# Optimization experiments

Hardware: AMD Instinct MI355X
Metric: run time of the kernel (lower is better)

## Reference

```python
import jax, jax.numpy as jnp
import numpy as np

HEAD_NUM = 8
EMB_SIZE = 768
B, N = 8, 1024


def setup_inputs() -> dict:
    key = jax.random.key(0)
    ks = jax.random.split(key, 9)
    s = 0.02
    return {
        "x": jax.random.normal(ks[0], (B, N, EMB_SIZE), dtype=jnp.float32),
        "Wq": jax.random.normal(ks[1], (EMB_SIZE, EMB_SIZE), dtype=jnp.float32) * s,
        "bq": jax.random.normal(ks[2], (EMB_SIZE,), dtype=jnp.float32) * s,
        "Wk": jax.random.normal(ks[3], (EMB_SIZE, EMB_SIZE), dtype=jnp.float32) * s,
        "bk": jax.random.normal(ks[4], (EMB_SIZE,), dtype=jnp.float32) * s,
        "Wv": jax.random.normal(ks[5], (EMB_SIZE, EMB_SIZE), dtype=jnp.float32) * s,
        "bv": jax.random.normal(ks[6], (EMB_SIZE,), dtype=jnp.float32) * s,
        "Wp": jax.random.normal(ks[7], (EMB_SIZE, EMB_SIZE), dtype=jnp.float32) * s,
        "bp": jax.random.normal(ks[8], (EMB_SIZE,), dtype=jnp.float32) * s,
    }


def reference(x, Wq, bq, Wk, bk, Wv, bv, Wp, bp):
    b, n, e = x.shape
    h = HEAD_NUM
    d = e // h
    # nn.Linear: y = x @ W^T + b
    q = (x @ Wq.T + bq).reshape(b, h, n, d)  # NOTE: raw reshape, as in source
    k = (x @ Wk.T + bk).reshape(b, h, n, d)
    v = (x @ Wv.T + bv).reshape(b, h, n, d)
    energy = jnp.einsum('bhqd,bhkd->bhqk', q, k)
    # source divides by sqrt(emb_size) AFTER softmax (faithful)
    attn = jax.nn.softmax(energy, axis=-1) / jnp.sqrt(jnp.float32(e))
    out = jnp.einsum('bhql,bhld->bhqd', attn, v).reshape(b, n, h * d)
    return out @ Wp.T + bp
```

## Files before the change

### kernel.cpp

```cpp
#include <hip/hip_runtime.h>
#include <hip/hip_bf16.h>


typedef __attribute__((ext_vector_type(8))) short short8;
typedef __attribute__((ext_vector_type(4))) float floatx4;
typedef __attribute__((ext_vector_type(16))) float floatx16;

static constexpr int EMB = 768;
static constexpr int SEQ = 1024;
static constexpr int DH = 96;
static constexpr int NBH = 64;
static constexpr int HEADBLK = SEQ * DH;
static constexpr int MROWS = 8192;
static constexpr int NW = EMB * EMB;
static constexpr int QKVN = 3 * EMB;

__device__ __forceinline__ unsigned bfround(float f) {
    unsigned u = __builtin_bit_cast(unsigned, f);
    return u + 0x7FFFu + ((u >> 16) & 1u);
}
__device__ __forceinline__ unsigned short f2bf(float f) {
    return (unsigned short)(bfround(f) >> 16);
}
__device__ __forceinline__ unsigned pk2(float lo, float hi) {
    return (bfround(lo) >> 16) | (bfround(hi) & 0xFFFF0000u);
}

__device__ __forceinline__ void gload16(const unsigned short* g, unsigned short* l) {
    __builtin_amdgcn_global_load_lds(
        (const __attribute__((address_space(1))) unsigned int*)g,
        (__attribute__((address_space(3))) unsigned int*)l, 16, 0, 0);
}

__global__ void cast_all(const float* __restrict__ x,
                         const float* __restrict__ Wq, const float* __restrict__ Wk,
                         const float* __restrict__ Wv, const float* __restrict__ Wp,
                         const float* __restrict__ bq, const float* __restrict__ bk,
                         const float* __restrict__ bv,
                         unsigned short* __restrict__ xb,
                         unsigned short* __restrict__ Wqkv, unsigned short* __restrict__ Wpb,
                         float* __restrict__ bias) {
    int bx = blockIdx.x;
    if (bx < 6144) {
        int i = bx * 1024 + threadIdx.x * 4;
        float4 v = *reinterpret_cast<const float4*>(x + i);
        ushort4 o;
        o.x = f2bf(v.x); o.y = f2bf(v.y); o.z = f2bf(v.z); o.w = f2bf(v.w);
        *reinterpret_cast<ushort4*>(xb + i) = o;
    } else if (bx < 8448) {
        int i4 = (bx - 6144) * 1024 + threadIdx.x * 4;
        const float* src;
        unsigned short* dst;
        if (i4 < 3 * NW) {
            int wi = i4 / NW;
            src = (wi == 0) ? Wq + i4 : (wi == 1) ? Wk + (i4 - NW) : Wv + (i4 - 2 * NW);
            dst = Wqkv + i4;
        } else {
            src = Wp + (i4 - 3 * NW);
            dst = Wpb + (i4 - 3 * NW);
        }
        float4 v = *reinterpret_cast<const float4*>(src);
        ushort4 o;
        o.x = f2bf(v.x); o.y = f2bf(v.y); o.z = f2bf(v.z); o.w = f2bf(v.w);
        *reinterpret_cast<ushort4*>(dst) = o;
    } else {
        int j = (bx - 8448) * 256 + threadIdx.x;
        if (j < QKVN)
            bias[j] = (j < 768) ? bq[j] : (j < 1536) ? bk[j - 768] : bv[j - 1536];
    }
}

__global__ __launch_bounds__(256) void gemm_qkv(
    const unsigned short* __restrict__ A,
    const unsigned short* __restrict__ Bm,
    const float* __restrict__ bias,
    unsigned short* __restrict__ Qo,
    unsigned short* __restrict__ Ko,
    unsigned short* __restrict__ Vo) {
    __shared__ unsigned short As[128 * 64];
    __shared__ unsigned short Bs[128 * 64];
    const int K = EMB;

    const int t = threadIdx.x;
    const int lane = t & 63;
    const int w = t >> 6;
    const int wm = (w >> 1) * 64;
    const int wn = (w & 1) * 64;
    const int l32 = lane & 31;
    const int lh = lane >> 5;
    const int bm = blockIdx.x * 128;
    const int by = blockIdx.y;
    const int bn = by * 128;

    const unsigned short* Agp[4];
    const unsigned short* Bgp[4];
#pragma unroll
    for (int i = 0; i < 4; i++) {
        int f = i * 2048 + w * 512 + lane * 8;
        int row = f >> 6;
        int cc = (f >> 3) & 7;
        int gk = (cc ^ (row & 7)) * 8;
        Agp[i] = A + (size_t)(bm + row) * K + gk;
        Bgp[i] = Bm + (size_t)(bn + row) * K + gk;
    }

    floatx16 acc[2][2];
#pragma unroll
    for (int i = 0; i < 2; i++)
#pragma unroll
        for (int j = 0; j < 2; j++)
#pragma unroll
            for (int r = 0; r < 16; r++) acc[i][j][r] = 0.0f;

    const int sx = lane & 7;
    for (int k0 = 0; k0 < K; k0 += 64) {
        __syncthreads();
#pragma unroll
        for (int i = 0; i < 4; i++) {
            gload16(Agp[i] + k0, As + i * 2048 + w * 512);
            gload16(Bgp[i] + k0, Bs + i * 2048 + w * 512);
        }
        __syncthreads();

#pragma unroll
        for (int ks = 0; ks < 4; ks++) {
            const int co = ((ks * 2 + lh) ^ sx) * 8;
            short8 af[2], bfr[2];
#pragma unroll
            for (int mt = 0; mt < 2; mt++)
                af[mt] = *reinterpret_cast<const short8*>(As + (wm + mt * 32 + l32) * 64 + co);
#pragma unroll
            for (int nt = 0; nt < 2; nt++)
                bfr[nt] = *reinterpret_cast<const short8*>(Bs + (wn + nt * 32 + l32) * 64 + co);
#pragma unroll
            for (int mt = 0; mt < 2; mt++)
#pragma unroll
                for (int nt = 0; nt < 2; nt++)
                    acc[mt][nt] = __builtin_amdgcn_mfma_f32_32x32x16_bf16(af[mt], bfr[nt], acc[mt][nt], 0, 0, 0);
        }
    }

    unsigned short* dst = (by < 6) ? Qo : (by < 12) ? Ko : Vo;
    const int bnl = (by % 6) * 128;
#pragma unroll
    for (int mt = 0; mt < 2; mt++) {
#pragma unroll
        for (int nt = 0; nt < 2; nt++) {
            int colg = bn + wn + nt * 32 + l32;
            int coll = bnl + wn + nt * 32 + l32;
            float bb = bias[colg];
#pragma unroll
            for (int rg = 0; rg < 4; rg++) {
                int rowb = bm + wm + mt * 32 + rg * 8 + lh * 4;
#pragma unroll
                for (int rr = 0; rr < 4; rr++)
                    dst[(size_t)(rowb + rr) * EMB + coll] = f2bf(acc[mt][nt][rg * 4 + rr] + bb);
            }
        }
    }
}

__global__ __launch_bounds__(256) void gemm_proj(
    const unsigned short* __restrict__ A,
    const unsigned short* __restrict__ Bm,
    const float* __restrict__ bias,
    float* __restrict__ C) {
    __shared__ unsigned short As[64 * 64];
    __shared__ unsigned short Bs[128 * 64];
    const int K = EMB, N = EMB;

    const int t = threadIdx.x;
    const int lane = t & 63;
    const int w = t >> 6;
    const int wm = (w >> 1) * 32;
    const int wn = (w & 1) * 64;
    const int l32 = lane & 31;
    const int lh = lane >> 5;
    const int bm = blockIdx.x * 64;
    const int bn = blockIdx.y * 128;

    const unsigned short* Agp[2];
    const unsigned short* Bgp[4];
#pragma unroll
    for (int i = 0; i < 2; i++) {
        int f = i * 2048 + w * 512 + lane * 8;
        int row = f >> 6;
        int cc = (f >> 3) & 7;
        Agp[i] = A + (size_t)(bm + row) * K + ((cc ^ (row & 7)) * 8);
    }
#pragma unroll
    for (int i = 0; i < 4; i++) {
        int f = i * 2048 + w * 512 + lane * 8;
        int row = f >> 6;
        int cc = (f >> 3) & 7;
        Bgp[i] = Bm + (size_t)(bn + row) * K + ((cc ^ (row & 7)) * 8);
    }

    floatx16 acc[2];
#pragma unroll
    for (int j = 0; j < 2; j++)
#pragma unroll
        for (int r = 0; r < 16; r++) acc[j][r] = 0.0f;

    const int sx = lane & 7;
    for (int k0 = 0; k0 < K; k0 += 64) {
        __syncthreads();
#pragma unroll
        for (int i = 0; i < 2; i++) gload16(Agp[i] + k0, As + i * 2048 + w * 512);
#pragma unroll
        for (int i = 0; i < 4; i++) gload16(Bgp[i] + k0, Bs + i * 2048 + w * 512);
        __syncthreads();

#pragma unroll
        for (int ks = 0; ks < 4; ks++) {
            const int co = ((ks * 2 + lh) ^ sx) * 8;
            short8 af = *reinterpret_cast<const short8*>(As + (wm + l32) * 64 + co);
            short8 bfr[2];
#pragma unroll
            for (int nt = 0; nt < 2; nt++)
                bfr[nt] = *reinterpret_cast<const short8*>(Bs + (wn + nt * 32 + l32) * 64 + co);
#pragma unroll
            for (int nt = 0; nt < 2; nt++)
                acc[nt] = __builtin_amdgcn_mfma_f32_32x32x16_bf16(af, bfr[nt], acc[nt], 0, 0, 0);
        }
    }

#pragma unroll
    for (int nt = 0; nt < 2; nt++) {
        int col = bn + wn + nt * 32 + l32;
        float bb = bias[col];
#pragma unroll
        for (int rg = 0; rg < 4; rg++) {
            int rowb = bm + wm + rg * 8 + lh * 4;
#pragma unroll
            for (int rr = 0; rr < 4; rr++)
                C[(size_t)(rowb + rr) * N + col] = acc[nt][rg * 4 + rr] + bb;
        }
    }
}

__global__ __launch_bounds__(256) void transpose_v(const unsigned short* __restrict__ V,
                                                   unsigned short* __restrict__ Vt) {
    __shared__ unsigned short L[64 * 104];
    const int t = threadIdx.x;
    const int bh = blockIdx.x, nb = blockIdx.y;
    const unsigned short* Vg = V + (size_t)bh * HEADBLK + (size_t)nb * 64 * DH;
#pragma unroll
    for (int i = 0; i < 3; i++) {
        int f = i * 2048 + t * 8;
        int r = f / 96, c = f - r * 96;
        *reinterpret_cast<short8*>(L + r * 104 + c) = *reinterpret_cast<const short8*>(Vg + f);
    }
    __syncthreads();
    unsigned short* dst = Vt + (size_t)bh * HEADBLK;
#pragma unroll
    for (int i = 0; i < 3; i++) {
        int f = i * 2048 + t * 8;
        int d = f >> 6, c0 = f & 63;
        union { short8 s; unsigned short u[8]; } o;
#pragma unroll
        for (int j = 0; j < 8; j++) {
            int c = c0 + j;
            int key = (c & ~12) | ((c & 4) << 1) | ((c & 8) >> 1);
            o.u[j] = L[key * 104 + d];
        }
        *reinterpret_cast<short8*>(dst + d * SEQ + nb * 64 + c0) = o.s;
    }
}

__global__ __launch_bounds__(256, 2) void attn_kernel(
    const unsigned short* __restrict__ Q,
    const unsigned short* __restrict__ K,
    const unsigned short* __restrict__ Vt,
    unsigned short* __restrict__ O) {
    __shared__ unsigned short Ks[64 * 104];
    __shared__ unsigned short Vs[96 * 72];

    const int t = threadIdx.x;
    const int lane = t & 63;
    const int w = t >> 6;
    const int l32 = lane & 31;
    const int lh = lane >> 5;
    const int bh = blockIdx.x, qb = blockIdx.y;

    const unsigned short* Qh = Q + (size_t)bh * HEADBLK;
    const unsigned short* Kh = K + (size_t)bh * HEADBLK;
    const unsigned short* Vth = Vt + (size_t)bh * HEADBLK;

    short8 qf[6];
    {
        const unsigned short* qsrc = Qh + (size_t)(qb * 128 + w * 32 + l32) * DH + lh * 8;
#pragma unroll
        for (int ks = 0; ks < 6; ks++)
            qf[ks] = *reinterpret_cast<const short8*>(qsrc + ks * 16);
    }

    const unsigned short* Kp[3];
    const unsigned short* Vp[3];
    unsigned short* KsW[3];
    unsigned short* VsW[3];
#pragma unroll
    for (int i = 0; i < 3; i++) {
        int f = i * 2048 + t * 8;
        int r = f / 96, c = f - r * 96;
        Kp[i] = Kh + f;
        KsW[i] = Ks + r * 104 + c;
        int d = f >> 6, cv = f & 63;
        Vp[i] = Vth + d * SEQ + cv;
        VsW[i] = Vs + d * 72 + cv;
    }

    short8 kreg[3], vreg[3];
#pragma unroll
    for (int i = 0; i < 3; i++) {
        kreg[i] = *reinterpret_cast<const short8*>(Kp[i]);
        vreg[i] = *reinterpret_cast<const short8*>(Vp[i]);
    }

    float l_ = 0.0f;
    floatx16 acco[3];
#pragma unroll
    for (int n = 0; n < 3; n++)
#pragma unroll
        for (int r = 0; r < 16; r++) acco[n][r] = 0.0f;

    for (int kb = 0; kb < 16; kb++) {
        __syncthreads();
#pragma unroll
        for (int i = 0; i < 3; i++) {
            *reinterpret_cast<short8*>(KsW[i]) = kreg[i];
            *reinterpret_cast<short8*>(VsW[i]) = vreg[i];
        }
        __syncthreads();
        if (kb < 15) {
#pragma unroll
            for (int i = 0; i < 3; i++) {
                kreg[i] = *reinterpret_cast<const short8*>(Kp[i] + (kb + 1) * 6144);
                vreg[i] = *reinterpret_cast<const short8*>(Vp[i] + (kb + 1) * 64);
            }
        }

        floatx16 sacc[2];
#pragma unroll
        for (int kt = 0; kt < 2; kt++)
#pragma unroll
            for (int r = 0; r < 16; r++) sacc[kt][r] = 0.0f;

#pragma unroll
        for (int ks = 0; ks < 6; ks++) {
#pragma unroll
            for (int kt = 0; kt < 2; kt++) {
                short8 ak = *reinterpret_cast<const short8*>(
                    Ks + (kt * 32 + l32) * 104 + ks * 16 + lh * 8);
                sacc[kt] = __builtin_amdgcn_mfma_f32_32x32x16_bf16(ak, qf[ks], sacc[kt], 0, 0, 0);
            }
        }

        float rs = 0.0f;
#pragma unroll
        for (int kt = 0; kt < 2; kt++)
#pragma unroll
            for (int r = 0; r < 16; r++) {
                float v = __expf(sacc[kt][r]);
                sacc[kt][r] = v;
                rs += v;
            }
        rs += __shfl_xor(rs, 32);
        l_ += rs;

#pragma unroll
        for (int kt2 = 0; kt2 < 4; kt2++) {
            const int kt = kt2 >> 1, ro = (kt2 & 1) * 8;
            union { short8 s8; unsigned u[4]; } bp;
#pragma unroll
            for (int p = 0; p < 4; p++)
                bp.u[p] = pk2(sacc[kt][ro + 2 * p], sacc[kt][ro + 2 * p + 1]);
#pragma unroll
            for (int n = 0; n < 3; n++) {
                short8 av = *reinterpret_cast<const short8*>(
                    Vs + (n * 32 + l32) * 72 + kt2 * 16 + lh * 8);
                acco[n] = __builtin_amdgcn_mfma_f32_32x32x16_bf16(av, bp.s8, acco[n], 0, 0, 0);
            }
        }
    }

    const float inv_sqrt_e = 0.036084391824351615f;
    float invl = inv_sqrt_e / l_;
    unsigned short* dst = O + (size_t)bh * HEADBLK +
                          (size_t)(qb * 128 + w * 32 + l32) * DH + lh * 4;
#pragma unroll
    for (int n = 0; n < 3; n++) {
#pragma unroll
        for (int rg = 0; rg < 4; rg++) {
            uint2 o2;
            o2.x = pk2(acco[n][rg * 4 + 0] * invl, acco[n][rg * 4 + 1] * invl);
            o2.y = pk2(acco[n][rg * 4 + 2] * invl, acco[n][rg * 4 + 3] * invl);
            *reinterpret_cast<uint2*>(dst + n * 32 + rg * 8) = o2;
        }
    }
}

extern "C" void kernel_launch(void* const* d_in, const int* in_sizes, int n_in,
                              void* d_out, int out_size, void* d_ws, size_t ws_size,
                              hipStream_t stream) {
    const float* x = (const float*)d_in[0];
    const float* Wq = (const float*)d_in[1];
    const float* bq = (const float*)d_in[2];
    const float* Wk = (const float*)d_in[3];
    const float* bk = (const float*)d_in[4];
    const float* Wv = (const float*)d_in[5];
    const float* bv = (const float*)d_in[6];
    const float* Wp = (const float*)d_in[7];
    const float* bp = (const float*)d_in[8];
    float* out = (float*)d_out;

    char* ws = (char*)d_ws;
    size_t off = 0;
    auto alloc = [&](size_t bytes) {
        char* p = ws + off;
        off += (bytes + 255) & ~(size_t)255;
        return p;
    };
    const int nx = MROWS * EMB;
    unsigned short* xb    = (unsigned short*)alloc((size_t)nx * 2);
    unsigned short* Wqkvb = (unsigned short*)alloc((size_t)3 * NW * 2);
    unsigned short* Wpb   = (unsigned short*)alloc((size_t)NW * 2);
    float*          biasq = (float*)alloc((size_t)QKVN * 4);
    unsigned short* Qb    = (unsigned short*)alloc((size_t)nx * 2);
    unsigned short* Kb    = (unsigned short*)alloc((size_t)nx * 2);
    unsigned short* Vb    = (unsigned short*)alloc((size_t)nx * 2);
    unsigned short* Vtb   = (unsigned short*)alloc((size_t)nx * 2);
    unsigned short* Ob    = (unsigned short*)alloc((size_t)nx * 2);

    cast_all<<<8457, 256, 0, stream>>>(x, Wq, Wk, Wv, Wp, bq, bk, bv,
                                       xb, Wqkvb, Wpb, biasq);

    gemm_qkv<<<dim3(MROWS / 128, QKVN / 128), 256, 0, stream>>>(
        xb, Wqkvb, biasq, Qb, Kb, Vb);

    transpose_v<<<dim3(NBH, SEQ / 64), 256, 0, stream>>>(Vb, Vtb);

    attn_kernel<<<dim3(NBH, SEQ / 128), 256, 0, stream>>>(Qb, Kb, Vtb, Ob);

    gemm_proj<<<dim3(MROWS / 64, EMB / 128), 256, 0, stream>>>(Ob, Wpb, bp, out);
}
```

Before: 188.7 us.

## Triple-buffer QKV GEMM with async global-to-LDS loads and 128x256 tiles

Rewrites the QKV projection GEMM to use 512-thread blocks computing 128x256 output tiles, with a three-stage LDS ring fed by asynchronous global loads two k-steps ahead. Explicit vmcnt waits plus one barrier per step replace the old two-barrier load-then-compute loop. All fragments of a k-step are loaded before an MFMA burst issued at raised priority. The aim is to hide global latency and reduce sync overhead, at the cost of a larger LDS footprint (about 144KB per block) and higher register pressure, which can limit occupancy.

```diff
diff --git a/kernel.cpp b/kernel.cpp
--- a/kernel.cpp
+++ b/kernel.cpp
@@ -70,38 +70,40 @@
     }
 }
 
-__global__ __launch_bounds__(256) void gemm_qkv(
+__global__ __launch_bounds__(512, 2) void gemm_qkv(
     const unsigned short* __restrict__ A,
     const unsigned short* __restrict__ Bm,
     const float* __restrict__ bias,
     unsigned short* __restrict__ Qo,
     unsigned short* __restrict__ Ko,
     unsigned short* __restrict__ Vo) {
-    __shared__ unsigned short As[128 * 64];
-    __shared__ unsigned short Bs[128 * 64];
-    const int K = EMB;
+    __shared__ unsigned short lds[3 * 24576];
 
     const int t = threadIdx.x;
     const int lane = t & 63;
     const int w = t >> 6;
-    const int wm = (w >> 1) * 64;
-    const int wn = (w & 1) * 64;
+    const int wm = (w >> 2) * 64;
+    const int wn = (w & 3) * 64;
     const int l32 = lane & 31;
     const int lh = lane >> 5;
+    const int sx = l32 & 7;
     const int bm = blockIdx.x * 128;
     const int by = blockIdx.y;
-    const int bn = by * 128;
-
-    const unsigned short* Agp[4];
+    const int bn = by * 256;
+
+    const unsigned short* Agp[2];
     const unsigned short* Bgp[4];
 #pragma unroll
+    for (int i = 0; i < 2; i++) {
+        int f = i * 512 + w * 64 + lane;
+        int row = f >> 3, cc = f & 7;
+        Agp[i] = A + (size_t)(bm + row) * EMB + ((cc ^ (row & 7)) * 8);
+    }
+#pragma unroll
     for (int i = 0; i < 4; i++) {
-        int f = i * 2048 + w * 512 + lane * 8;
-        int row = f >> 6;
-        int cc = (f >> 3) & 7;
-        int gk = (cc ^ (row & 7)) * 8;
-        Agp[i] = A + (size_t)(bm + row) * K + gk;
-        Bgp[i] = Bm + (size_t)(bn + row) * K + gk;
+        int f = i * 512 + w * 64 + lane;
+        int row = f >> 3, cc = f & 7;
+        Bgp[i] = Bm + (size_t)(bn + row) * EMB + ((cc ^ (row & 7)) * 8);
     }
 
     floatx16 acc[2][2];
@@ -112,36 +114,61 @@
 #pragma unroll
             for (int r = 0; r < 16; r++) acc[i][j][r] = 0.0f;
 
-    const int sx = lane & 7;
-    for (int k0 = 0; k0 < K; k0 += 64) {
-        __syncthreads();
-#pragma unroll
-        for (int i = 0; i < 4; i++) {
-            gload16(Agp[i] + k0, As + i * 2048 + w * 512);
-            gload16(Bgp[i] + k0, Bs + i * 2048 + w * 512);
-        }
-        __syncthreads();
-
+    auto stage = [&](int tt, int b) {
+        unsigned short* Ab = lds + b * 24576;
+        unsigned short* Bb = Ab + 8192;
+        const int ko = tt * 64;
+#pragma unroll
+        for (int i = 0; i < 2; i++)
+            gload16(Agp[i] + ko, Ab + i * 4096 + w * 512);
+#pragma unroll
+        for (int i = 0; i < 4; i++)
+            gload16(Bgp[i] + ko, Bb + i * 4096 + w * 512);
+    };
+
+    stage(0, 0);
+    stage(1, 1);
+
+#pragma unroll
+    for (int tt = 0; tt < 12; tt++) {
+        if (tt == 11) {
+            asm volatile("s_waitcnt vmcnt(0)" ::: "memory");
+        } else {
+            asm volatile("s_waitcnt vmcnt(6)" ::: "memory");
+        }
+        __builtin_amdgcn_s_barrier();
+        __builtin_amdgcn_sched_barrier(0);
+        if (tt + 2 < 12) stage(tt + 2, (tt + 2) % 3);
+
+        const unsigned short* Ab = lds + (tt % 3) * 24576;
+        const unsigned short* Bb = Ab + 8192;
+        short8 af[4][2], bfq[4][2];
 #pragma unroll
         for (int ks = 0; ks < 4; ks++) {
             const int co = ((ks * 2 + lh) ^ sx) * 8;
-            short8 af[2], bfr[2];
 #pragma unroll
             for (int mt = 0; mt < 2; mt++)
-                af[mt] = *reinterpret_cast<const short8*>(As + (wm + mt * 32 + l32) * 64 + co);
+                af[ks][mt] = *reinterpret_cast<const short8*>(
+                    Ab + (wm + mt * 32 + l32) * 64 + co);
 #pragma unroll
             for (int nt = 0; nt < 2; nt++)
-                bfr[nt] = *reinterpret_cast<const short8*>(Bs + (wn + nt * 32 + l32) * 64 + co);
+                bfq[ks][nt] = *reinterpret_cast<const short8*>(
+                    Bb + (wn + nt * 32 + l32) * 64 + co);
+        }
+        __builtin_amdgcn_s_setprio(1);
+#pragma unroll
+        for (int ks = 0; ks < 4; ks++)
 #pragma unroll
             for (int mt = 0; mt < 2; mt++)
 #pragma unroll
                 for (int nt = 0; nt < 2; nt++)
-                    acc[mt][nt] = __builtin_amdgcn_mfma_f32_32x32x16_bf16(af[mt], bfr[nt], acc[mt][nt], 0, 0, 0);
-        }
-    }
-
-    unsigned short* dst = (by < 6) ? Qo : (by < 12) ? Ko : Vo;
-    const int bnl = (by % 6) * 128;
+                    acc[mt][nt] = __builtin_amdgcn_mfma_f32_32x32x16_bf16(
+                        af[ks][mt], bfq[ks][nt], acc[mt][nt], 0, 0, 0);
+        __builtin_amdgcn_s_setprio(0);
+    }
+
+    unsigned short* dst = (by < 3) ? Qo : (by < 6) ? Ko : Vo;
+    const int bnl = (by % 3) * 256;
 #pragma unroll
     for (int mt = 0; mt < 2; mt++) {
 #pragma unroll
@@ -435,7 +462,7 @@
     cast_all<<<8457, 256, 0, stream>>>(x, Wq, Wk, Wv, Wp, bq, bk, bv,
                                        xb, Wqkvb, Wpb, biasq);
 
-    gemm_qkv<<<dim3(MROWS / 128, QKVN / 128), 256, 0, stream>>>(
+    gemm_qkv<<<dim3(MROWS / 128, QKVN / 256), 512, 0, stream>>>(
         xb, Wqkvb, biasq, Qb, Kb, Vb);
 
     transpose_v<<<dim3(NBH, SEQ / 64), 256, 0, stream>>>(Vb, Vtb);
```

New measurement: 197.6 us. +4.8%, slower.

## Load K and V fragments directly from global memory, dropping LDS staging

Applied to the files above, without the earlier changes.

The attention kernel no longer stages K and V tiles through shared memory with two barriers per key block. Each wave now loads its own MFMA operand fragments for K (prefetched one block ahead) and V straight from global memory into registers. This removes LDS traffic and the __syncthreads calls. In exchange, each of the four waves re-reads the same K/V data from global memory or cache, and register pressure rises with 24 extra short8 fragments, which may hurt occupancy.

```diff
diff --git a/kernel.cpp b/kernel.cpp
--- a/kernel.cpp
+++ b/kernel.cpp
@@ -273,9 +273,6 @@
     const unsigned short* __restrict__ K,
     const unsigned short* __restrict__ Vt,
     unsigned short* __restrict__ O) {
-    __shared__ unsigned short Ks[64 * 104];
-    __shared__ unsigned short Vs[96 * 72];
-
     const int t = threadIdx.x;
     const int lane = t & 63;
     const int w = t >> 6;
@@ -295,27 +292,8 @@
             qf[ks] = *reinterpret_cast<const short8*>(qsrc + ks * 16);
     }
 
-    const unsigned short* Kp[3];
-    const unsigned short* Vp[3];
-    unsigned short* KsW[3];
-    unsigned short* VsW[3];
-#pragma unroll
-    for (int i = 0; i < 3; i++) {
-        int f = i * 2048 + t * 8;
-        int r = f / 96, c = f - r * 96;
-        Kp[i] = Kh + f;
-        KsW[i] = Ks + r * 104 + c;
-        int d = f >> 6, cv = f & 63;
-        Vp[i] = Vth + d * SEQ + cv;
-        VsW[i] = Vs + d * 72 + cv;
-    }
-
-    short8 kreg[3], vreg[3];
-#pragma unroll
-    for (int i = 0; i < 3; i++) {
-        kreg[i] = *reinterpret_cast<const short8*>(Kp[i]);
-        vreg[i] = *reinterpret_cast<const short8*>(Vp[i]);
-    }
+    const unsigned short* kp = Kh + (size_t)l32 * DH + lh * 8;
+    const unsigned short* vp = Vth + (size_t)l32 * SEQ + lh * 8;
 
     float l_ = 0.0f;
     floatx16 acco[3];
@@ -324,36 +302,41 @@
 #pragma unroll
         for (int r = 0; r < 16; r++) acco[n][r] = 0.0f;
 
+    short8 kf[12];
+#pragma unroll
+    for (int kt = 0; kt < 2; kt++)
+#pragma unroll
+        for (int ks = 0; ks < 6; ks++)
+            kf[kt * 6 + ks] = *reinterpret_cast<const short8*>(kp + (kt * 32) * DH + ks * 16);
+
     for (int kb = 0; kb < 16; kb++) {
-        __syncthreads();
-#pragma unroll
-        for (int i = 0; i < 3; i++) {
-            *reinterpret_cast<short8*>(KsW[i]) = kreg[i];
-            *reinterpret_cast<short8*>(VsW[i]) = vreg[i];
-        }
-        __syncthreads();
+        floatx16 sacc[2];
+#pragma unroll
+        for (int kt = 0; kt < 2; kt++)
+#pragma unroll
+            for (int r = 0; r < 16; r++) sacc[kt][r] = 0.0f;
+#pragma unroll
+        for (int ks = 0; ks < 6; ks++)
+#pragma unroll
+            for (int kt = 0; kt < 2; kt++)
+                sacc[kt] = __builtin_amdgcn_mfma_f32_32x32x16_bf16(
+                    kf[kt * 6 + ks], qf[ks], sacc[kt], 0, 0, 0);
+
+        short8 vf[12];
+#pragma unroll
+        for (int n = 0; n < 3; n++)
+#pragma unroll
+            for (int kt2 = 0; kt2 < 4; kt2++)
+                vf[n * 4 + kt2] = *reinterpret_cast<const short8*>(
+                    vp + (size_t)(n * 32) * SEQ + kb * 64 + kt2 * 16);
+
         if (kb < 15) {
 #pragma unroll
-            for (int i = 0; i < 3; i++) {
-                kreg[i] = *reinterpret_cast<const short8*>(Kp[i] + (kb + 1) * 6144);
-                vreg[i] = *reinterpret_cast<const short8*>(Vp[i] + (kb + 1) * 64);
-            }
-        }
-
-        floatx16 sacc[2];
-#pragma unroll
-        for (int kt = 0; kt < 2; kt++)
-#pragma unroll
-            for (int r = 0; r < 16; r++) sacc[kt][r] = 0.0f;
-
-#pragma unroll
-        for (int ks = 0; ks < 6; ks++) {
-#pragma unroll
-            for (int kt = 0; kt < 2; kt++) {
-                short8 ak = *reinterpret_cast<const short8*>(
-                    Ks + (kt * 32 + l32) * 104 + ks * 16 + lh * 8);
-                sacc[kt] = __builtin_amdgcn_mfma_f32_32x32x16_bf16(ak, qf[ks], sacc[kt], 0, 0, 0);
-            }
+            for (int kt = 0; kt < 2; kt++)
+#pragma unroll
+                for (int ks = 0; ks < 6; ks++)
+                    kf[kt * 6 + ks] = *reinterpret_cast<const short8*>(
+                        kp + ((kb + 1) * 64 + kt * 32) * DH + ks * 16);
         }
 
         float rs = 0.0f;
@@ -376,11 +359,9 @@
             for (int p = 0; p < 4; p++)
                 bp.u[p] = pk2(sacc[kt][ro + 2 * p], sacc[kt][ro + 2 * p + 1]);
 #pragma unroll
-            for (int n = 0; n < 3; n++) {
-                short8 av = *reinterpret_cast<const short8*>(
-                    Vs + (n * 32 + l32) * 72 + kt2 * 16 + lh * 8);
-                acco[n] = __builtin_amdgcn_mfma_f32_32x32x16_bf16(av, bp.s8, acco[n], 0, 0, 0);
-            }
+            for (int n = 0; n < 3; n++)
+                acco[n] = __builtin_amdgcn_mfma_f32_32x32x16_bf16(
+                    vf[n * 4 + kt2], bp.s8, acco[n], 0, 0, 0);
         }
     }
 
```

Result: slower. 220.9 us (+17.1%).
